# Optimization experiments

Measured on AMD Instinct MI355X. Metric: run time of the kernel, lower is better.

## Reference

```python
import jax, jax.numpy as jnp
import numpy as np

BATCH = 32
NUM_ANCHORS = 3
NUM_CLASSES = 80
GRID = 52
INP_DIM = 416


def setup_inputs() -> dict:
    key = jax.random.key(0)
    k1, _ = jax.random.split(key)
    prediction = jax.random.normal(
        k1, (BATCH, NUM_ANCHORS * (5 + NUM_CLASSES), GRID, GRID), dtype=jnp.float32)
    anchors = jnp.array([[10.0, 13.0], [16.0, 30.0], [33.0, 23.0]], dtype=jnp.float32)
    return {"prediction": prediction, "anchors": anchors,
            "inp_dim": INP_DIM, "num_classes": NUM_CLASSES}


def reference(prediction, anchors, inp_dim, num_classes):
    # YOLOv3 detection-head decode (targets=None inference path).
    B = prediction.shape[0]
    G = prediction.shape[2]
    stride = inp_dim // G
    A = anchors.shape[0]
    attrs = 5 + num_classes

    # [B, A, attrs, G, G] -> [B, A, G, G, attrs]  (grid dims are (gj, gi))
    p = prediction.reshape(B, A, attrs, G, G).transpose(0, 1, 3, 4, 2)

    anc = anchors / stride  # anchors in grid units, [A, 2]

    xy = jax.nn.sigmoid(p[..., 0:2])          # sigmoid(tx), sigmoid(ty)
    conf = jax.nn.sigmoid(p[..., 4:5])
    cls = jax.nn.sigmoid(p[..., 5:])

    g = jnp.arange(G, dtype=p.dtype)
    x_off = g.reshape(1, 1, 1, G)   # varies along gi (last spatial axis)
    y_off = g.reshape(1, 1, G, 1)   # varies along gj

    # Torch code detaches x/y/w/h before decoding into box coords.
    bx = jax.lax.stop_gradient(xy[..., 0]) + x_off
    by = jax.lax.stop_gradient(xy[..., 1]) + y_off
    bw = jnp.exp(jax.lax.stop_gradient(p[..., 2])) * anc[:, 0].reshape(1, A, 1, 1)
    bh = jnp.exp(jax.lax.stop_gradient(p[..., 3])) * anc[:, 1].reshape(1, A, 1, 1)

    coords = jnp.stack([bx, by, bw, bh], axis=-1) * stride  # back to pixel units
    pred = jnp.concatenate([coords, conf, cls], axis=-1)    # [B, A, G, G, attrs]
    # permute(0,2,3,1,4).view(B, G*G*A, attrs)
    pred = pred.transpose(0, 2, 3, 1, 4).reshape(B, G * G * A, attrs)
    return pred
```

## Files before the change

### kernel.cpp

```cpp
#include <hip/hip_runtime.h>
#include <math.h>


#define GG 52
#define NROWS 255
#define PLANE 2704
#define NGRP 5408
#define L2E 1.442695040889f

typedef float f32x4 __attribute__((ext_vector_type(4)));

__device__ __forceinline__ float fast_sigmoid(float x) {
    return __builtin_amdgcn_rcpf(1.0f + __builtin_amdgcn_exp2f(-L2E * x));
}

__global__ __launch_bounds__(256, 8)
void detect_decode_kernel(const float* __restrict__ in,
                          const float* __restrict__ anchors,
                          float* __restrict__ out) {
    __shared__ float tile[16 * NROWS];

    const int B   = blockIdx.x;
    const int g   = (B & 7) * (NGRP / 8) + (B >> 3);
    const int b   = g / 169;
    const int s0  = (g - b * 169) * 16;
    const int t   = threadIdx.x;

    const float* __restrict__ src = in + (size_t)b * NROWS * PLANE + s0;

    #pragma unroll
    for (int it = 0; it < 4; ++it) {
        const int idx = t + it * 256;
        if (idx < NROWS * 4) {
            const int c = idx >> 2;
            const int q = idx & 3;
            const f32x4 v = *reinterpret_cast<const f32x4*>(
                src + (size_t)c * PLANE + 4 * q);
            const int e = (4 * q) * NROWS + c;
            tile[e            ] = v.x;
            tile[e +     NROWS] = v.y;
            tile[e + 2 * NROWS] = v.z;
            tile[e + 3 * NROWS] = v.w;
        }
    }

    __syncthreads();

    const float a0x = anchors[0], a0y = anchors[1];
    const float a1x = anchors[2], a1y = anchors[3];
    const float a2x = anchors[4], a2y = anchors[5];

    float* __restrict__ dst = out + ((size_t)b * PLANE + s0) * NROWS;

    #pragma unroll
    for (int it = 0; it < 4; ++it) {
        const int i = t + it * 256;
        if (i < NROWS * 4) {
            const f32x4 u = *reinterpret_cast<const f32x4*>(&tile[4 * i]);
            const int e0  = 4 * i;

            float r[4];
            #pragma unroll
            for (int k = 0; k < 4; ++k) {
                const int e   = e0 + k;
                const int s_l = e / NROWS;
                const int c   = e - s_l * NROWS;
                const int a    = (c >= 170) ? 2 : (c >= 85 ? 1 : 0);
                const int attr = c - a * 85;
                const int s    = s0 + s_l;
                const int gj   = s / GG;
                const int gi   = s - gj * GG;

                const float x  = (k == 0) ? u.x : (k == 1) ? u.y
                               : (k == 2) ? u.z : u.w;
                const float sg = fast_sigmoid(x);
                const float ex = __builtin_amdgcn_exp2f(L2E * x);
                const float ancx = (a == 0) ? a0x : (a == 1) ? a1x : a2x;
                const float ancy = (a == 0) ? a0y : (a == 1) ? a1y : a2y;

                float r_;
                if (attr >= 4)      r_ = sg;
                else if (attr == 0) r_ = (sg + (float)gi) * 8.0f;
                else if (attr == 1) r_ = (sg + (float)gj) * 8.0f;
                else if (attr == 2) r_ = ex * ancx;
                else                r_ = ex * ancy;
                r[k] = r_;
            }

            f32x4 o; o.x = r[0]; o.y = r[1]; o.z = r[2]; o.w = r[3];
            __builtin_nontemporal_store(o, reinterpret_cast<f32x4*>(dst + 4 * i));
        }
    }
}

extern "C" void kernel_launch(void* const* d_in, const int* in_sizes, int n_in,
                              void* d_out, int out_size, void* d_ws, size_t ws_size,
                              hipStream_t stream) {
    const float* pred    = (const float*)d_in[0];
    const float* anchors = (const float*)d_in[1];
    float* out = (float*)d_out;

    detect_decode_kernel<<<NGRP, 256, 0, stream>>>(pred, anchors, out);
}
```

Baseline: 38.44 us.

## Decode in load phase with channel-uniform branching and branchless clamped store

Moves the sigmoid/exp decode into the global-load phase, where each thread's channel index is fixed. Only sigmoid is computed on the common path, and the box-coordinate math (grid offsets, exp times anchor) sits behind a rarely taken branch. The old per-element divisions and double transcendental evaluation in the store phase go away, so that phase becomes a pure LDS-to-global copy. The bounds checks are replaced by index clamping, which makes some threads redundantly write duplicate data. The nontemporal store hint is also dropped.

```diff
diff --git a/kernel.cpp b/kernel.cpp
--- a/kernel.cpp
+++ b/kernel.cpp
@@ -20,77 +20,85 @@
                           float* __restrict__ out) {
     __shared__ float tile[16 * NROWS];
 
-    const int B   = blockIdx.x;
-    const int g   = (B & 7) * (NGRP / 8) + (B >> 3);
-    const int b   = g / 169;
-    const int s0  = (g - b * 169) * 16;
-    const int t   = threadIdx.x;
+    const int B    = blockIdx.x;
+    const int g    = (B & 7) * (NGRP / 8) + (B >> 3);
+    const int b    = g / 169;
+    const int s0   = (g - b * 169) * 16;
+    const int gj0  = s0 / GG;
+    const int rem0 = s0 - gj0 * GG;
+    const int t    = threadIdx.x;
 
     const float* __restrict__ src = in + (size_t)b * NROWS * PLANE + s0;
-
-    #pragma unroll
-    for (int it = 0; it < 4; ++it) {
-        const int idx = t + it * 256;
-        if (idx < NROWS * 4) {
-            const int c = idx >> 2;
-            const int q = idx & 3;
-            const f32x4 v = *reinterpret_cast<const f32x4*>(
-                src + (size_t)c * PLANE + 4 * q);
-            const int e = (4 * q) * NROWS + c;
-            tile[e            ] = v.x;
-            tile[e +     NROWS] = v.y;
-            tile[e + 2 * NROWS] = v.z;
-            tile[e + 3 * NROWS] = v.w;
-        }
-    }
-
-    __syncthreads();
 
     const float a0x = anchors[0], a0y = anchors[1];
     const float a1x = anchors[2], a1y = anchors[3];
     const float a2x = anchors[4], a2y = anchors[5];
 
+    #pragma unroll
+    for (int it = 0; it < 4; ++it) {
+        int idx = t + it * 256;
+        if (idx > 1019) idx = 1019;
+        const int c = idx >> 2;
+        const int q = idx & 3;
+
+        const f32x4 v = *reinterpret_cast<const f32x4*>(
+            src + (size_t)c * PLANE + 4 * q);
+
+        f32x4 r;
+        r.x = fast_sigmoid(v.x);
+        r.y = fast_sigmoid(v.y);
+        r.z = fast_sigmoid(v.z);
+        r.w = fast_sigmoid(v.w);
+
+        const bool sp0 = c < 4;
+        const bool sp1 = (unsigned)(c - 85)  < 4u;
+        const bool sp2 = (unsigned)(c - 170) < 4u;
+        if (__builtin_expect(sp0 | sp1 | sp2, 0)) {
+            const int attr = sp0 ? c : (sp1 ? c - 85 : c - 170);
+            const float ancx = sp0 ? a0x : (sp1 ? a1x : a2x);
+            const float ancy = sp0 ? a0y : (sp1 ? a1y : a2y);
+            const float anc  = (attr == 2) ? ancx : ancy;
+            #pragma unroll
+            for (int k = 0; k < 4; ++k) {
+                const int rem = rem0 + 4 * q + k;
+                const int wv  = (rem >= GG) ? 1 : 0;
+                const int gi  = rem - (wv ? GG : 0);
+                const int gj  = gj0 + wv;
+                const float x  = v[k];
+                const float sg = r[k];
+                float rr;
+                if (attr == 0)      rr = (sg + (float)gi) * 8.0f;
+                else if (attr == 1) rr = (sg + (float)gj) * 8.0f;
+                else                rr = __builtin_amdgcn_exp2f(L2E * x) * anc;
+                r[k] = rr;
+            }
+        }
+
+        const int e = q * 4 * NROWS + c;
+        tile[e            ] = r.x;
+        tile[e +     NROWS] = r.y;
+        tile[e + 2 * NROWS] = r.z;
+        tile[e + 3 * NROWS] = r.w;
+    }
+
+    __syncthreads();
+
     float* __restrict__ dst = out + ((size_t)b * PLANE + s0) * NROWS;
 
-    #pragma unroll
-    for (int it = 0; it < 4; ++it) {
-        const int i = t + it * 256;
-        if (i < NROWS * 4) {
-            const f32x4 u = *reinterpret_cast<const f32x4*>(&tile[4 * i]);
-            const int e0  = 4 * i;
+    const int i0 = t;
+    const int i1 = t + 256;
+    const int i2 = t + 512;
+    const int i3 = (t + 768 < 1020) ? t + 768 : 1019;
 
-            float r[4];
-            #pragma unroll
-            for (int k = 0; k < 4; ++k) {
-                const int e   = e0 + k;
-                const int s_l = e / NROWS;
-                const int c   = e - s_l * NROWS;
-                const int a    = (c >= 170) ? 2 : (c >= 85 ? 1 : 0);
-                const int attr = c - a * 85;
-                const int s    = s0 + s_l;
-                const int gj   = s / GG;
-                const int gi   = s - gj * GG;
+    const f32x4 u0 = *reinterpret_cast<const f32x4*>(&tile[4 * i0]);
+    const f32x4 u1 = *reinterpret_cast<const f32x4*>(&tile[4 * i1]);
+    const f32x4 u2 = *reinterpret_cast<const f32x4*>(&tile[4 * i2]);
+    const f32x4 u3 = *reinterpret_cast<const f32x4*>(&tile[4 * i3]);
 
-                const float x  = (k == 0) ? u.x : (k == 1) ? u.y
-                               : (k == 2) ? u.z : u.w;
-                const float sg = fast_sigmoid(x);
-                const float ex = __builtin_amdgcn_exp2f(L2E * x);
-                const float ancx = (a == 0) ? a0x : (a == 1) ? a1x : a2x;
-                const float ancy = (a == 0) ? a0y : (a == 1) ? a1y : a2y;
-
-                float r_;
-                if (attr >= 4)      r_ = sg;
-                else if (attr == 0) r_ = (sg + (float)gi) * 8.0f;
-                else if (attr == 1) r_ = (sg + (float)gj) * 8.0f;
-                else if (attr == 2) r_ = ex * ancx;
-                else                r_ = ex * ancy;
-                r[k] = r_;
-            }
-
-            f32x4 o; o.x = r[0]; o.y = r[1]; o.z = r[2]; o.w = r[3];
-            __builtin_nontemporal_store(o, reinterpret_cast<f32x4*>(dst + 4 * i));
-        }
-    }
+    *reinterpret_cast<f32x4*>(dst + 4 * i0) = u0;
+    *reinterpret_cast<f32x4*>(dst + 4 * i1) = u1;
+    *reinterpret_cast<f32x4*>(dst + 4 * i2) = u2;
+    *reinterpret_cast<f32x4*>(dst + 4 * i3) = u3;
 }
 
 extern "C" void kernel_launch(void* const* d_in, const int* in_sizes, int n_in,
```

New measurement: 31.53 us. 18.0% less time.
